# Optimization experiments

Measured on AMD Instinct MI355X. Metric: run time of the kernel, lower is better.

Reference implementation:

```python
import jax, jax.numpy as jnp
import numpy as np

N_NODES = 100000
N_EDGES = 1000000
M_DIM = 4
HID = 64
N_GRAPHS = 64


def setup_inputs() -> dict:
    key = jax.random.key(0)
    ks = jax.random.split(key, 16)
    x = jax.random.normal(ks[0], (N_NODES, 1, M_DIM), dtype=jnp.float32)
    edge_index = jax.random.randint(ks[1], (2, N_EDGES), 0, N_NODES, dtype=jnp.int64)
    batch = jnp.sort(jax.random.randint(ks[2], (N_NODES,), 0, N_GRAPHS, dtype=jnp.int64))
    def lin(k, out_c, in_c):
        bound = 1.0 / np.sqrt(in_c)
        return jax.random.uniform(k, (out_c, in_c), jnp.float32, -bound, bound)
    inp = {"x": x, "edge_index": edge_index, "batch": batch}
    inp["W1l"] = lin(ks[3], HID, 1); inp["b1l"] = jnp.zeros((HID,), jnp.float32)
    inp["W1r"] = lin(ks[4], HID, 1)
    inp["W2l"] = lin(ks[5], HID, HID); inp["b2l"] = jnp.zeros((HID,), jnp.float32)
    inp["W2r"] = lin(ks[6], HID, HID)
    inp["W3l"] = lin(ks[7], HID, HID); inp["b3l"] = jnp.zeros((HID,), jnp.float32)
    inp["W3r"] = lin(ks[8], HID, HID)
    inp["Wlin"] = lin(ks[9], 1, HID); inp["blin"] = jnp.zeros((1,), jnp.float32)
    return inp


def _sage_conv(x, src, dst, Wl, bl, Wr):
    # x: [N, F, M]; mean aggregation over in-edges, then lin_l/lin_r GEMMs.
    N, F, M = x.shape
    msg = x[src]  # [E, F, M] gather
    s = jax.ops.segment_sum(msg, dst, num_segments=N)
    cnt = jax.ops.segment_sum(jnp.ones((src.shape[0],), x.dtype), dst, num_segments=N)
    agg = s / jnp.maximum(cnt, 1.0)[:, None, None]  # [N, F, M]
    C = Wl.shape[0]
    # torch .view(N*M, F) on contiguous [N,F,M] == row-major reshape (mixes F and M)
    h = (agg.reshape(N * M, F) @ Wl.T + bl).reshape(N, C, M)
    h = h + (x.reshape(N * M, F) @ Wr.T).reshape(N, C, M)
    return h


def reference(x, edge_index, batch, W1l, b1l, W1r, W2l, b2l, W2r, W3l, b3l, W3r, Wlin, blin):
    src, dst = edge_index[0], edge_index[1]
    h = jax.nn.relu(_sage_conv(x, src, dst, W1l, b1l, W1r))
    h = jax.nn.relu(_sage_conv(h, src, dst, W2l, b2l, W2r))
    h = jax.nn.relu(_sage_conv(h, src, dst, W3l, b3l, W3r))
    # new_global_mean_pool: scatter-mean over nodes -> [B, HID, M]
    sums = jax.ops.segment_sum(h, batch, num_segments=N_GRAPHS)
    cnts = jax.ops.segment_sum(jnp.ones((h.shape[0],), h.dtype), batch, num_segments=N_GRAPHS)
    pooled = sums / jnp.maximum(cnts, 1.0)[:, None, None]
    # dropout in eval mode == identity
    B, F, M = pooled.shape
    z = (pooled.reshape(B * M, F) @ Wlin.T + blin).reshape(B, M)
    return jax.nn.sigmoid(z).mean(axis=1)  # [B]
```

## Files before the change

### kernel.cpp

```cpp
#include <hip/hip_runtime.h>
#include <math.h>

#define TPB 256

typedef unsigned short ushort_t;
typedef unsigned char uchar_t;
typedef __attribute__((ext_vector_type(8))) short short8v;
typedef __attribute__((ext_vector_type(4))) float f32x4;
typedef __attribute__((ext_vector_type(8))) unsigned short ushort8;

__device__ __forceinline__ float b2f(unsigned short u) {
  union { unsigned int i; float f; } c; c.i = ((unsigned int)u) << 16; return c.f;
}
__device__ __forceinline__ unsigned short f2b(float f) {
  union { float f; unsigned int i; } c; c.f = f;
  unsigned int x = c.i;
  x += 0x7FFFu + ((x >> 16) & 1u);
  return (unsigned short)(x >> 16);
}

__device__ __forceinline__ short8v fp8x8_to_bf16(const uchar_t* p) {
  uint2 u = *(const uint2*)p;
  auto p0 = __builtin_amdgcn_cvt_pk_f32_fp8(u.x, false);
  auto p1 = __builtin_amdgcn_cvt_pk_f32_fp8(u.x, true);
  auto p2 = __builtin_amdgcn_cvt_pk_f32_fp8(u.y, false);
  auto p3 = __builtin_amdgcn_cvt_pk_f32_fp8(u.y, true);
  ushort8 o;
  o[0] = f2b(p0[0]); o[1] = f2b(p0[1]); o[2] = f2b(p1[0]); o[3] = f2b(p1[1]);
  o[4] = f2b(p2[0]); o[5] = f2b(p2[1]); o[6] = f2b(p3[0]); o[7] = f2b(p3[1]);
  union { ushort8 a; short8v b; } c; c.a = o; return c.b;
}

__global__ void k_hist(const int* __restrict__ dst, int* deg, int E) {
  int e = blockIdx.x * TPB + threadIdx.x;
  if (e < E) atomicAdd(&deg[dst[e]], 1);
}

__global__ void k_gcnt(const int* __restrict__ batch, int* gcnt, int N) {
  int t = blockIdx.x * TPB + threadIdx.x;
  int n0 = t * 16;
  if (n0 >= N) return;
  int n1 = min(n0 + 16, N);
  int cur = batch[n0];
  int c = 0;
  for (int n = n0; n < n1; ++n) {
    int b = batch[n];
    if (b != cur) { atomicAdd(&gcnt[cur], c); cur = b; c = 0; }
    ++c;
  }
  atomicAdd(&gcnt[cur], c);
}

__global__ void k_scan1(const int* __restrict__ deg, int* rp, int* bsum, int N) {
  __shared__ int s[TPB];
  int t = threadIdx.x;
  int i = blockIdx.x * TPB + t;
  int v = (i < N) ? ((deg[i] + 7) & ~7) : 0;
  s[t] = v;
  __syncthreads();
  for (int d = 1; d < TPB; d <<= 1) {
    int u = (t >= d) ? s[t - d] : 0;
    __syncthreads();
    s[t] += u;
    __syncthreads();
  }
  if (i < N) rp[i] = s[t] - v;
  if (t == TPB - 1) bsum[blockIdx.x] = s[t];
}

__global__ void k_scan2(const int* bsum, int* boff, int nb) {
  __shared__ int s[1024];
  int t = threadIdx.x;
  int v = (t < nb) ? bsum[t] : 0;
  s[t] = v;
  __syncthreads();
  for (int d = 1; d < 1024; d <<= 1) {
    int u = (t >= d) ? s[t - d] : 0;
    __syncthreads();
    s[t] += u;
    __syncthreads();
  }
  if (t < nb) boff[t] = s[t] - v;
}

__global__ void k_scan3(int* rp, const int* __restrict__ boff, const int* __restrict__ bsum,
                        int* cursor, int N, int nb) {
  int i = blockIdx.x * TPB + threadIdx.x;
  if (i < N) {
    int v = rp[i] + boff[i >> 8];
    rp[i] = v;
    cursor[i] = v;
  } else if (i == N) {
    rp[N] = boff[nb - 1] + bsum[nb - 1];
  }
}

__global__ void k_fill(const int* __restrict__ src, const int* __restrict__ dst,
                       int* cursor, int* __restrict__ csr, int E) {
  int e = blockIdx.x * TPB + threadIdx.x;
  if (e < E) {
    int p = atomicAdd(&cursor[dst[e]], 1);
    csr[p] = src[e];
  }
}

__global__ void k_pad(const int* __restrict__ cursor, const int* __restrict__ rp,
                      int* __restrict__ csr, int N) {
  int n = blockIdx.x * TPB + threadIdx.x;
  if (n >= N) return;
  int c = cursor[n], e = rp[n + 1];
  for (int p = c; p < e; ++p) csr[p] = N;
}

__global__ void k_cvtw(const float* __restrict__ s0, const float* __restrict__ s1,
                       const float* __restrict__ s2, const float* __restrict__ s3,
                       ushort_t* d0, ushort_t* d1, ushort_t* d2, ushort_t* d3, int n) {
  int i = blockIdx.x * TPB + threadIdx.x;
  if (i < n) { d0[i] = f2b(s0[i]); d1[i] = f2b(s1[i]); d2[i] = f2b(s2[i]); d3[i] = f2b(s3[i]); }
}

__global__ void k_agg1(const float4* __restrict__ x, const int* __restrict__ rp,
                       const int* __restrict__ deg, const int* __restrict__ csr,
                       float4* __restrict__ agg1, int N) {
  int n = blockIdx.x * TPB + threadIdx.x;
  if (n >= N) return;
  int b = rp[n], d = deg[n], e = b + d;
  float4 a = make_float4(0.f, 0.f, 0.f, 0.f);
  int i = b;
  for (; i + 1 < e; i += 2) {
    float4 v0 = x[csr[i]];
    float4 v1 = x[csr[i + 1]];
    a.x += v0.x + v1.x; a.y += v0.y + v1.y;
    a.z += v0.z + v1.z; a.w += v0.w + v1.w;
  }
  if (i < e) {
    float4 v = x[csr[i]];
    a.x += v.x; a.y += v.y; a.z += v.z; a.w += v.w;
  }
  float inv = (d > 0) ? 1.f / (float)d : 0.f;
  a.x *= inv; a.y *= inv; a.z *= inv; a.w *= inv;
  agg1[n] = a;
}

__global__ void k_l1(const float* __restrict__ x, const float* __restrict__ agg1,
                     const float* __restrict__ W1l, const float* __restrict__ b1l,
                     const float* __restrict__ W1r, ushort_t* __restrict__ h,
                     uchar_t* __restrict__ h8, int rows) {
  int q = blockIdx.x * TPB + threadIdx.x;
  if (q >= rows * 8) return;
  int r = q >> 3, c8 = (q & 7) * 8;
  float a = agg1[r], xx = x[r];
  float vv[8];
  ushort8 o;
#pragma unroll
  for (int k = 0; k < 8; ++k) {
    vv[k] = fmaxf(a * W1l[c8 + k] + b1l[c8 + k] + xx * W1r[c8 + k], 0.f);
    o[k] = f2b(vv[k]);
  }
  *(ushort8*)(h + (size_t)r * 64 + c8) = o;
  unsigned int w0 = __builtin_amdgcn_cvt_pk_fp8_f32(vv[0], vv[1], 0u, false);
  w0 = __builtin_amdgcn_cvt_pk_fp8_f32(vv[2], vv[3], w0, true);
  unsigned int w1 = __builtin_amdgcn_cvt_pk_fp8_f32(vv[4], vv[5], 0u, false);
  w1 = __builtin_amdgcn_cvt_pk_fp8_f32(vv[6], vv[7], w1, true);
  uint2 st; st.x = w0; st.y = w1;
  *(uint2*)(h8 + (size_t)r * 64 + c8) = st;
}

#define NB1(IDX) { \
    uint4 v = *(const uint4*)(h8sl + (size_t)(IDX) * 256); \
    auto q0 = __builtin_amdgcn_cvt_pk_f32_fp8(v.x, false); \
    auto q1 = __builtin_amdgcn_cvt_pk_f32_fp8(v.x, true);  \
    auto q2 = __builtin_amdgcn_cvt_pk_f32_fp8(v.y, false); \
    auto q3 = __builtin_amdgcn_cvt_pk_f32_fp8(v.y, true);  \
    auto q4 = __builtin_amdgcn_cvt_pk_f32_fp8(v.z, false); \
    auto q5 = __builtin_amdgcn_cvt_pk_f32_fp8(v.z, true);  \
    auto q6 = __builtin_amdgcn_cvt_pk_f32_fp8(v.w, false); \
    auto q7 = __builtin_amdgcn_cvt_pk_f32_fp8(v.w, true);  \
    acc[0] += q0[0];  acc[1] += q0[1];  acc[2] += q1[0];  acc[3] += q1[1];  \
    acc[4] += q2[0];  acc[5] += q2[1];  acc[6] += q3[0];  acc[7] += q3[1];  \
    acc[8] += q4[0];  acc[9] += q4[1];  acc[10] += q5[0]; acc[11] += q5[1]; \
    acc[12] += q6[0]; acc[13] += q6[1]; acc[14] += q7[0]; acc[15] += q7[1]; }

__global__ __launch_bounds__(256) void k_layer(
    const ushort_t* __restrict__ hInBf, const uchar_t* __restrict__ hIn8,
    const int* __restrict__ rp, const int* __restrict__ deg, const int* __restrict__ csr,
    const ushort_t* __restrict__ Wlb, const ushort_t* __restrict__ Wrb,
    const float* __restrict__ bias, ushort_t* __restrict__ hOut,
    uchar_t* __restrict__ hOut8, int N) {
  __shared__ ushort_t As[8192];
  __shared__ __align__(16) int csr_s[16 * 68];
  int t = threadIdx.x;
  int wave = t >> 6, lane = t & 63;
  int g = lane >> 4, l15 = lane & 15;
  int gq = t >> 4, li = t & 15;
  int n0 = blockIdx.x * 32;
  int r0 = blockIdx.x * 128;

  const uchar_t* h8sl = hIn8 + li * 16;

  int nb0 = n0 + gq * 2;
  int gb = rp[nb0];
  int cnt = rp[nb0 + 2] - gb;
  bool fits = (cnt <= 64);
  if (fits) {
    for (int i = li; i < cnt; i += 16) csr_s[gq * 68 + i] = csr[gb + i];
  }

#pragma unroll
  for (int k2 = 0; k2 < 2; ++k2) {
    int nl = gq * 2 + k2;
    int n = n0 + nl;
    int b = rp[n], e = rp[n + 1];
    float acc[16];
#pragma unroll
    for (int j = 0; j < 16; ++j) acc[j] = 0.f;

    if (fits) {
      for (int i = b - gb; i < e - gb; i += 8) {
        int4 c0 = *(const int4*)&csr_s[gq * 68 + i];
        int4 c1 = *(const int4*)&csr_s[gq * 68 + i + 4];
        NB1(c0.x) NB1(c0.y) NB1(c0.z) NB1(c0.w)
        NB1(c1.x) NB1(c1.y) NB1(c1.z) NB1(c1.w)
      }
    } else {
      for (int i = b; i < e; i += 8) {
        int4 c0 = *(const int4*)(csr + i);
        int4 c1 = *(const int4*)(csr + i + 4);
        NB1(c0.x) NB1(c0.y) NB1(c0.z) NB1(c0.w)
        NB1(c1.x) NB1(c1.y) NB1(c1.z) NB1(c1.w)
      }
    }

    int d = deg[n];
    float inv = (d > 0) ? 1.f / (float)d : 0.f;
    ushort8 pk0, pk1;
#pragma unroll
    for (int j = 0; j < 8; ++j) {
      pk0[j] = f2b(acc[j] * inv);
      pk1[j] = f2b(acc[j + 8] * inv);
    }
    int row = nl * 4 + (li >> 2);
    int cb = (li & 3) * 32;
    int xr = (row & 7) << 4;
    *(ushort8*)((char*)As + row * 128 + (cb ^ xr)) = pk0;
    *(ushort8*)((char*)As + row * 128 + ((cb + 16) ^ xr)) = pk1;
  }
  __syncthreads();

  short8v af[2][2], hf[2][2];
#pragma unroll
  for (int tile = 0; tile < 2; ++tile) {
    int arow = wave * 32 + tile * 16 + l15;
    int xr = (arow & 7) << 4;
    af[tile][0] = *(const short8v*)((char*)As + arow * 128 + ((g * 16) ^ xr));
    af[tile][1] = *(const short8v*)((char*)As + arow * 128 + ((g * 16 + 64) ^ xr));
    int rbase = r0 + arow;
    if (hInBf) {
      const ushort_t* hrow = hInBf + (size_t)rbase * 64;
      hf[tile][0] = *(const short8v*)(hrow + g * 8);
      hf[tile][1] = *(const short8v*)(hrow + 32 + g * 8);
    } else {
      const uchar_t* hrow8 = hIn8 + (size_t)rbase * 64;
      hf[tile][0] = fp8x8_to_bf16(hrow8 + g * 8);
      hf[tile][1] = fp8x8_to_bf16(hrow8 + 32 + g * 8);
    }
  }

  f32x4 fac[4][2];
#pragma unroll
  for (int c = 0; c < 4; ++c) {
    float bv = bias[c * 16 + l15];
    const ushort_t* wl = Wlb + (size_t)(c * 16 + l15) * 64;
    const ushort_t* wr = Wrb + (size_t)(c * 16 + l15) * 64;
    short8v bl0 = *(const short8v*)(wl + g * 8);
    short8v bl1 = *(const short8v*)(wl + 32 + g * 8);
    short8v br0 = *(const short8v*)(wr + g * 8);
    short8v br1 = *(const short8v*)(wr + 32 + g * 8);
#pragma unroll
    for (int tile = 0; tile < 2; ++tile) {
      fac[c][tile] = (f32x4){bv, bv, bv, bv};
      fac[c][tile] = __builtin_amdgcn_mfma_f32_16x16x32_bf16(af[tile][0], bl0, fac[c][tile], 0, 0, 0);
      fac[c][tile] = __builtin_amdgcn_mfma_f32_16x16x32_bf16(af[tile][1], bl1, fac[c][tile], 0, 0, 0);
      fac[c][tile] = __builtin_amdgcn_mfma_f32_16x16x32_bf16(hf[tile][0], br0, fac[c][tile], 0, 0, 0);
      fac[c][tile] = __builtin_amdgcn_mfma_f32_16x16x32_bf16(hf[tile][1], br1, fac[c][tile], 0, 0, 0);
    }
  }

  bool wBf = (hOut != nullptr);
  bool wF8 = (hOut8 != nullptr);
#pragma unroll
  for (int tile = 0; tile < 2; ++tile) {
#pragma unroll
    for (int c = 0; c < 4; ++c) {
#pragma unroll
      for (int i2 = 0; i2 < 4; ++i2) {
        int grow = r0 + wave * 32 + tile * 16 + g * 4 + i2;
        float v = fmaxf(fac[c][tile][i2], 0.f);
        size_t off = (size_t)grow * 64 + c * 16 + l15;
        if (wBf) hOut[off] = f2b(v);
        if (wF8) hOut8[off] =
            (uchar_t)(__builtin_amdgcn_cvt_pk_fp8_f32(v, v, 0u, false) & 0xFF);
      }
    }
  }
}

__global__ void k_pool(const ushort_t* __restrict__ h, const int* __restrict__ batch,
                       float* pooled, int N) {
  int t = threadIdx.x;
  int nPer = (N + gridDim.x - 1) / gridDim.x;
  int n0 = blockIdx.x * nPer;
  int n1 = min(N, n0 + nPer);
  if (n0 >= n1) return;
  float acc = 0.f;
  int cur = batch[n0];
  for (int n = n0; n < n1; ++n) {
    int b = batch[n];
    if (b != cur) {
      atomicAdd(&pooled[cur * 256 + t], acc);
      acc = 0.f;
      cur = b;
    }
    acc += b2f(h[(size_t)n * 256 + t]);
  }
  atomicAdd(&pooled[cur * 256 + t], acc);
}

__global__ void k_final(const float* __restrict__ pooled, const int* __restrict__ gcnt,
                        const float* __restrict__ Wlin, const float* __restrict__ blin,
                        float* __restrict__ out, int B) {
  int t = blockIdx.x * TPB + threadIdx.x;
  int b = t >> 2, j = t & 3;
  if (b >= B) return;
  float inv = 1.f / fmaxf((float)gcnt[b], 1.f);
  float s = blin[0];
  const float* p = pooled + b * 256 + j * 64;
#pragma unroll
  for (int f = 0; f < 64; ++f) s += p[f] * inv * Wlin[f];
  float z = 1.f / (1.f + expf(-s));
  z += __shfl_xor(z, 1);
  z += __shfl_xor(z, 2);
  if (j == 0) out[b] = 0.25f * z;
}

extern "C" void kernel_launch(void* const* d_in, const int* in_sizes, int n_in,
                              void* d_out, int out_size, void* d_ws, size_t ws_size,
                              hipStream_t stream) {
  const float* x   = (const float*)d_in[0];
  const int* edge  = (const int*)d_in[1];
  const int* batch = (const int*)d_in[2];
  const float* W1l = (const float*)d_in[3];
  const float* b1l = (const float*)d_in[4];
  const float* W1r = (const float*)d_in[5];
  const float* W2l = (const float*)d_in[6];
  const float* b2l = (const float*)d_in[7];
  const float* W2r = (const float*)d_in[8];
  const float* W3l = (const float*)d_in[9];
  const float* b3l = (const float*)d_in[10];
  const float* W3r = (const float*)d_in[11];
  const float* Wlin = (const float*)d_in[12];
  const float* blin = (const float*)d_in[13];
  float* out = (float*)d_out;

  const int N = in_sizes[0] / 4;
  const int E = in_sizes[1] / 2;
  const int B = out_size;
  const int rows = 4 * N;

  const int* srcA = edge;
  const int* dstA = edge + E;

  char* p = (char*)d_ws;
  auto carve = [&](size_t bytes) -> void* {
    void* r = (void*)p;
    p += (bytes + 255) & ~(size_t)255;
    return r;
  };
  int* deg     = (int*)carve((size_t)N * 4);
  int* rp      = (int*)carve((size_t)(N + 1) * 4);
  int* cursor  = (int*)carve((size_t)N * 4);
  int* bsum    = (int*)carve(4096);
  int* boff    = (int*)carve(4096);
  int* gcnt    = (int*)carve((size_t)B * 4);
  int* csr     = (int*)carve(((size_t)E + 8 * (size_t)N) * 4);
  float* agg1  = (float*)carve((size_t)N * 4 * 4);
  float* pooled = (float*)carve((size_t)B * 256 * 4);
  ushort_t* Wb2l = (ushort_t*)carve(4096 * 2);
  ushort_t* Wb2r = (ushort_t*)carve(4096 * 2);
  ushort_t* Wb3l = (ushort_t*)carve(4096 * 2);
  ushort_t* Wb3r = (ushort_t*)carve(4096 * 2);
  ushort_t* hA  = (ushort_t*)carve(((size_t)N + 1) * 256 * 2);
  uchar_t* hA8  = (uchar_t*)carve(((size_t)N + 1) * 256);
  uchar_t* hB8  = (uchar_t*)carve(((size_t)N + 1) * 256);
  (void)ws_size; (void)n_in;

  hipMemsetAsync(deg, 0, (size_t)N * 4, stream);
  hipMemsetAsync(gcnt, 0, (size_t)B * 4, stream);
  hipMemsetAsync(pooled, 0, (size_t)B * 256 * 4, stream);
  hipMemsetAsync(hA8 + (size_t)N * 256, 0, 256, stream);
  hipMemsetAsync(hB8 + (size_t)N * 256, 0, 256, stream);

  int nbScan = (N + TPB - 1) / TPB;

  k_hist<<<(E + TPB - 1) / TPB, TPB, 0, stream>>>(dstA, deg, E);
  k_gcnt<<<((N + 15) / 16 + TPB - 1) / TPB, TPB, 0, stream>>>(batch, gcnt, N);
  k_cvtw<<<16, TPB, 0, stream>>>(W2l, W2r, W3l, W3r, Wb2l, Wb2r, Wb3l, Wb3r, 4096);
  k_scan1<<<nbScan, TPB, 0, stream>>>(deg, rp, bsum, N);
  k_scan2<<<1, 1024, 0, stream>>>(bsum, boff, nbScan);
  k_scan3<<<(N + 1 + TPB - 1) / TPB, TPB, 0, stream>>>(rp, boff, bsum, cursor, N, nbScan);
  k_fill<<<(E + TPB - 1) / TPB, TPB, 0, stream>>>(srcA, dstA, cursor, csr, E);
  k_pad<<<(N + TPB - 1) / TPB, TPB, 0, stream>>>(cursor, rp, csr, N);

  k_agg1<<<(N + TPB - 1) / TPB, TPB, 0, stream>>>((const float4*)x, rp, deg, csr, (float4*)agg1, N);
  k_l1<<<((size_t)rows * 8 + TPB - 1) / TPB, TPB, 0, stream>>>(x, agg1, W1l, b1l, W1r, hA, hA8, rows);

  int nbLayer = (N + 31) / 32;
  k_layer<<<nbLayer, TPB, 0, stream>>>(hA, hA8, rp, deg, csr, Wb2l, Wb2r, b2l,
                                       (ushort_t*)nullptr, hB8, N);
  k_layer<<<nbLayer, TPB, 0, stream>>>((const ushort_t*)nullptr, hB8, rp, deg, csr,
                                       Wb3l, Wb3r, b3l, hA, (uchar_t*)nullptr, N);

  k_pool<<<512, TPB, 0, stream>>>(hA, batch, pooled, N);
  k_final<<<(B * 4 + TPB - 1) / TPB, TPB, 0, stream>>>(pooled, gcnt, Wlin, blin, out, B);
}
```

Baseline: 428.8 us.

## Interleave two nodes' neighbor gathers and unroll agg1 and pool loops

The layer kernel now processes the two nodes per thread group together. It loads eight padded neighbor indices for each node per iteration and accumulates into two accumulator sets, so twice as many independent fp8 gathers are in flight. k_agg1 reads the padded CSR in int4 chunks of eight and masks out the sentinel indices. k_pool is unrolled by four with a fast path when all four nodes share a graph, and its grid is doubled. The aim is more memory-level parallelism in gather-bound loops, at the cost of higher register pressure and redundant gathers when the two nodes' degrees differ.

```diff
diff --git a/kernel.cpp b/kernel.cpp
--- a/kernel.cpp
+++ b/kernel.cpp
@@ -124,19 +124,20 @@
                        float4* __restrict__ agg1, int N) {
   int n = blockIdx.x * TPB + threadIdx.x;
   if (n >= N) return;
-  int b = rp[n], d = deg[n], e = b + d;
+  int b = rp[n], e = rp[n + 1];
   float4 a = make_float4(0.f, 0.f, 0.f, 0.f);
-  int i = b;
-  for (; i + 1 < e; i += 2) {
-    float4 v0 = x[csr[i]];
-    float4 v1 = x[csr[i + 1]];
-    a.x += v0.x + v1.x; a.y += v0.y + v1.y;
-    a.z += v0.z + v1.z; a.w += v0.w + v1.w;
-  }
-  if (i < e) {
-    float4 v = x[csr[i]];
-    a.x += v.x; a.y += v.y; a.z += v.z; a.w += v.w;
-  }
+  for (int i = b; i < e; i += 8) {
+    int4 c0 = *(const int4*)(csr + i);
+    int4 c1 = *(const int4*)(csr + i + 4);
+    int id[8] = {c0.x, c0.y, c0.z, c0.w, c1.x, c1.y, c1.z, c1.w};
+#pragma unroll
+    for (int j = 0; j < 8; ++j) {
+      float4 v = x[min(id[j], N - 1)];
+      float m = (id[j] < N) ? 1.f : 0.f;
+      a.x += v.x * m; a.y += v.y * m; a.z += v.z * m; a.w += v.w * m;
+    }
+  }
+  int d = deg[n];
   float inv = (d > 0) ? 1.f / (float)d : 0.f;
   a.x *= inv; a.y *= inv; a.z *= inv; a.w *= inv;
   agg1[n] = a;
@@ -166,7 +167,7 @@
   *(uint2*)(h8 + (size_t)r * 64 + c8) = st;
 }
 
-#define NB1(IDX) { \
+#define NB8(ACC, IDX) { \
     uint4 v = *(const uint4*)(h8sl + (size_t)(IDX) * 256); \
     auto q0 = __builtin_amdgcn_cvt_pk_f32_fp8(v.x, false); \
     auto q1 = __builtin_amdgcn_cvt_pk_f32_fp8(v.x, true);  \
@@ -176,10 +177,10 @@
     auto q5 = __builtin_amdgcn_cvt_pk_f32_fp8(v.z, true);  \
     auto q6 = __builtin_amdgcn_cvt_pk_f32_fp8(v.w, false); \
     auto q7 = __builtin_amdgcn_cvt_pk_f32_fp8(v.w, true);  \
-    acc[0] += q0[0];  acc[1] += q0[1];  acc[2] += q1[0];  acc[3] += q1[1];  \
-    acc[4] += q2[0];  acc[5] += q2[1];  acc[6] += q3[0];  acc[7] += q3[1];  \
-    acc[8] += q4[0];  acc[9] += q4[1];  acc[10] += q5[0]; acc[11] += q5[1]; \
-    acc[12] += q6[0]; acc[13] += q6[1]; acc[14] += q7[0]; acc[15] += q7[1]; }
+    ACC[0] += q0[0];  ACC[1] += q0[1];  ACC[2] += q1[0];  ACC[3] += q1[1];  \
+    ACC[4] += q2[0];  ACC[5] += q2[1];  ACC[6] += q3[0];  ACC[7] += q3[1];  \
+    ACC[8] += q4[0];  ACC[9] += q4[1];  ACC[10] += q5[0]; ACC[11] += q5[1]; \
+    ACC[12] += q6[0]; ACC[13] += q6[1]; ACC[14] += q7[0]; ACC[15] += q7[1]; }
 
 __global__ __launch_bounds__(256) void k_layer(
     const ushort_t* __restrict__ hInBf, const uchar_t* __restrict__ hIn8,
@@ -198,47 +199,62 @@
 
   const uchar_t* h8sl = hIn8 + li * 16;
 
-  int nb0 = n0 + gq * 2;
-  int gb = rp[nb0];
-  int cnt = rp[nb0 + 2] - gb;
+  int nA = n0 + gq * 2;
+  int gb = rp[nA];
+  int eAabs = rp[nA + 1];
+  int cnt = rp[nA + 2] - gb;
   bool fits = (cnt <= 64);
   if (fits) {
     for (int i = li; i < cnt; i += 16) csr_s[gq * 68 + i] = csr[gb + i];
   }
 
+  int eA = eAabs - gb;
+  int itA = eA >> 3;
+  int itB = (cnt - eA) >> 3;
+  int itM = max(itA, itB);
+  int oCap = max(cnt - 8, 0);
+
+  float accA[16], accB[16];
+#pragma unroll
+  for (int j = 0; j < 16; ++j) { accA[j] = 0.f; accB[j] = 0.f; }
+
+  for (int it = 0; it < itM; ++it) {
+    int oA = min(8 * min(it, max(itA - 1, 0)), oCap);
+    int oB = min(eA + 8 * min(it, max(itB - 1, 0)), oCap);
+    bool vA = it < itA, vB = it < itB;
+    int4 a0, a1, b0, b1;
+    if (fits) {
+      a0 = *(const int4*)&csr_s[gq * 68 + oA];
+      a1 = *(const int4*)&csr_s[gq * 68 + oA + 4];
+      b0 = *(const int4*)&csr_s[gq * 68 + oB];
+      b1 = *(const int4*)&csr_s[gq * 68 + oB + 4];
+    } else {
+      a0 = *(const int4*)(csr + gb + oA);
+      a1 = *(const int4*)(csr + gb + oA + 4);
+      b0 = *(const int4*)(csr + gb + oB);
+      b1 = *(const int4*)(csr + gb + oB + 4);
+    }
+    if (!vA) { a0 = make_int4(N, N, N, N); a1 = a0; }
+    if (!vB) { b0 = make_int4(N, N, N, N); b1 = b0; }
+    NB8(accA, a0.x) NB8(accA, a0.y) NB8(accA, a0.z) NB8(accA, a0.w)
+    NB8(accA, a1.x) NB8(accA, a1.y) NB8(accA, a1.z) NB8(accA, a1.w)
+    NB8(accB, b0.x) NB8(accB, b0.y) NB8(accB, b0.z) NB8(accB, b0.w)
+    NB8(accB, b1.x) NB8(accB, b1.y) NB8(accB, b1.z) NB8(accB, b1.w)
+  }
+
 #pragma unroll
   for (int k2 = 0; k2 < 2; ++k2) {
-    int nl = gq * 2 + k2;
-    int n = n0 + nl;
-    int b = rp[n], e = rp[n + 1];
-    float acc[16];
-#pragma unroll
-    for (int j = 0; j < 16; ++j) acc[j] = 0.f;
-
-    if (fits) {
-      for (int i = b - gb; i < e - gb; i += 8) {
-        int4 c0 = *(const int4*)&csr_s[gq * 68 + i];
-        int4 c1 = *(const int4*)&csr_s[gq * 68 + i + 4];
-        NB1(c0.x) NB1(c0.y) NB1(c0.z) NB1(c0.w)
-        NB1(c1.x) NB1(c1.y) NB1(c1.z) NB1(c1.w)
-      }
-    } else {
-      for (int i = b; i < e; i += 8) {
-        int4 c0 = *(const int4*)(csr + i);
-        int4 c1 = *(const int4*)(csr + i + 4);
-        NB1(c0.x) NB1(c0.y) NB1(c0.z) NB1(c0.w)
-        NB1(c1.x) NB1(c1.y) NB1(c1.z) NB1(c1.w)
-      }
-    }
-
+    int n = nA + k2;
     int d = deg[n];
     float inv = (d > 0) ? 1.f / (float)d : 0.f;
+    float* acc = k2 ? accB : accA;
     ushort8 pk0, pk1;
 #pragma unroll
     for (int j = 0; j < 8; ++j) {
       pk0[j] = f2b(acc[j] * inv);
       pk1[j] = f2b(acc[j + 8] * inv);
     }
+    int nl = gq * 2 + k2;
     int row = nl * 4 + (li >> 2);
     int cb = (li & 3) * 32;
     int xr = (row & 7) << 4;
@@ -314,13 +330,30 @@
   if (n0 >= n1) return;
   float acc = 0.f;
   int cur = batch[n0];
-  for (int n = n0; n < n1; ++n) {
+  int n = n0;
+  for (; n + 3 < n1; n += 4) {
+    int b0 = batch[n], b3 = batch[n + 3];
+    float v0 = b2f(h[(size_t)n * 256 + t]);
+    float v1 = b2f(h[(size_t)(n + 1) * 256 + t]);
+    float v2 = b2f(h[(size_t)(n + 2) * 256 + t]);
+    float v3 = b2f(h[(size_t)(n + 3) * 256 + t]);
+    if (b0 == b3) {
+      if (b0 != cur) { atomicAdd(&pooled[cur * 256 + t], acc); acc = 0.f; cur = b0; }
+      acc += (v0 + v1) + (v2 + v3);
+    } else {
+      int bb1 = batch[n + 1], bb2 = batch[n + 2];
+      int bb[4] = {b0, bb1, bb2, b3};
+      float vv[4] = {v0, v1, v2, v3};
+#pragma unroll
+      for (int j = 0; j < 4; ++j) {
+        if (bb[j] != cur) { atomicAdd(&pooled[cur * 256 + t], acc); acc = 0.f; cur = bb[j]; }
+        acc += vv[j];
+      }
+    }
+  }
+  for (; n < n1; ++n) {
     int b = batch[n];
-    if (b != cur) {
-      atomicAdd(&pooled[cur * 256 + t], acc);
-      acc = 0.f;
-      cur = b;
-    }
+    if (b != cur) { atomicAdd(&pooled[cur * 256 + t], acc); acc = 0.f; cur = b; }
     acc += b2f(h[(size_t)n * 256 + t]);
   }
   atomicAdd(&pooled[cur * 256 + t], acc);
@@ -420,6 +453,6 @@
   k_layer<<<nbLayer, TPB, 0, stream>>>((const ushort_t*)nullptr, hB8, rp, deg, csr,
                                        Wb3l, Wb3r, b3l, hA, (uchar_t*)nullptr, N);
 
-  k_pool<<<512, TPB, 0, stream>>>(hA, batch, pooled, N);
+  k_pool<<<1024, TPB, 0, stream>>>(hA, batch, pooled, N);
   k_final<<<(B * 4 + TPB - 1) / TPB, TPB, 0, stream>>>(pooled, gcnt, Wlin, blin, out, B);
 }
```

Result: faster. 381.6 us (-11.0%).
